# Performance work log

Hardware: AMD Instinct MI355X
Metric: run time of the kernel (lower is better)

## Reference

```python
import jax, jax.numpy as jnp
from jax import lax
import numpy as np

CLASS_NUMBER = 19
REGION_RADIUS = 1
KERNEL = 2 * REGION_RADIUS + 1  # 3
IMAGE_TOPK = 256
EPS = 1e-6


def setup_inputs() -> dict:
    key = jax.random.key(0)
    # softmax-like probabilities over classes
    raw = jax.random.uniform(key, (4, CLASS_NUMBER, 512, 1024), dtype=jnp.float32)
    logit = raw / jnp.sum(raw, axis=1, keepdims=True)
    return {"logit": logit}


def _box_sum(x):
    # kxk box sum with zero padding (SAME for odd kernel == pad=radius)
    return lax.reduce_window(x, jnp.float32(0), lax.add,
                             (1, 1, KERNEL, KERNEL), (1, 1, 1, 1), 'SAME')


def reference(logit):
    B, C, H, W = logit.shape
    logC = jnp.log(jnp.float32(C))

    # region uncertainty: normalized entropy, then avg-pool (count_include_pad)
    entropy = jnp.sum(-logit * jnp.log(logit + EPS), axis=1, keepdims=True) / logC
    region_uncertainty = _box_sum(entropy) / (KERNEL * KERNEL)  # [B,1,H,W]

    # region impurity: argmax -> one-hot -> depthwise box-sum (ones kernel)
    predict = jnp.argmax(logit, axis=1)                       # [B,H,W]
    one_hot = jax.nn.one_hot(predict, C, axis=1, dtype=logit.dtype)  # [B,C,H,W]
    summary = _box_sum(one_hot)                               # [B,C,H,W]
    count = jnp.sum(summary, axis=1, keepdims=True)           # [B,1,H,W]
    dist = summary / count
    region_impurity = jnp.sum(-dist * jnp.log(dist + EPS), axis=1, keepdims=True) / logC

    score = region_uncertainty * region_impurity              # [B,1,H,W]

    # per-image score: sum of top-k region scores
    flat = score.reshape(B, H * W)
    topk_vals, _ = lax.top_k(flat, IMAGE_TOPK)
    image_score = jnp.sum(topk_vals, axis=1)                  # [B]
    return image_score
```

## Files before the change

kernel.cpp:

```cpp
#include <hip/hip_runtime.h>
#include <cstdint>
#include <cstddef>

#define BB 4
#define CC 19
#define HH 512
#define WW 1024
#define HW (HH*WW)
#define HW4 (HW/4)
#define BHW (BB*HW)
#define KTOP 256
#define EPSF 1e-6f
#define NB1 8192
#define SEG 128
#define LOGC 2.9444389791664403f

__device__ __forceinline__ unsigned int sortable(float x) {
    unsigned int u = __float_as_uint(x);
    return (u & 0x80000000u) ? ~u : (u | 0x80000000u);
}
__device__ __forceinline__ float unsortable(unsigned int K) {
    unsigned int u = (K & 0x80000000u) ? (K & 0x7FFFFFFFu) : ~K;
    return __uint_as_float(u);
}

__global__ __launch_bounds__(256) void k_ent(const float4* __restrict__ logit,
                                             float4* __restrict__ ent,
                                             uchar4* __restrict__ pred,
                                             unsigned int* __restrict__ histz) {
    int idx = blockIdx.x * 256 + threadIdx.x;
    if (idx < 65536) histz[idx] = 0;
    int b = idx >> 17;
    int q = idx & (HW4 - 1);
    const float4* base = logit + (size_t)b * CC * HW4 + q;
    float e0 = 0.f, e1 = 0.f, e2 = 0.f, e3 = 0.f;
    float m0 = -1.f, m1 = -1.f, m2 = -1.f, m3 = -1.f;
    int a0 = 0, a1 = 0, a2 = 0, a3 = 0;
#pragma unroll
    for (int c = 0; c < CC; ++c) {
        float4 p = base[(size_t)c * HW4];
        e0 -= p.x * __logf(p.x + EPSF); if (p.x > m0) { m0 = p.x; a0 = c; }
        e1 -= p.y * __logf(p.y + EPSF); if (p.y > m1) { m1 = p.y; a1 = c; }
        e2 -= p.z * __logf(p.z + EPSF); if (p.z > m2) { m2 = p.z; a2 = c; }
        e3 -= p.w * __logf(p.w + EPSF); if (p.w > m3) { m3 = p.w; a3 = c; }
    }
    ent[idx] = make_float4(e0, e1, e2, e3);
    pred[idx] = make_uchar4((unsigned char)a0, (unsigned char)a1,
                            (unsigned char)a2, (unsigned char)a3);
}

__global__ __launch_bounds__(256) void k_score_hist(const float* __restrict__ ent,
                                                    const unsigned char* __restrict__ pred,
                                                    float* __restrict__ score,
                                                    unsigned int* __restrict__ hist1) {
    __shared__ unsigned int lh[NB1];
    int b = blockIdx.x >> 7;
    int seg = blockIdx.x & (SEG - 1);
    for (int i = threadIdx.x; i < NB1; i += 256) lh[i] = 0;
    __syncthreads();
    const float* eb = ent + (size_t)b * HW;
    const unsigned char* pb = pred + (size_t)b * HW;
    int base = seg * (HW / SEG);

    for (int it = 0; it < 16; ++it) {
        int hw = base + it * 256 + threadIdx.x;
        int h = hw >> 10;
        int w = hw & (WW - 1);

        float es = 0.f;
        int cls[9];
        int nv = 0;
#pragma unroll
        for (int i = 0; i < 9; ++i) {
            int dh = i / 3 - 1, dw = i % 3 - 1;
            int hh = h + dh, ww = w + dw;
            bool ok = (hh >= 0) & (hh < HH) & (ww >= 0) & (ww < WW);
            int o = ok ? ((hh << 10) | ww) : 0;
            es += ok ? eb[o] : 0.f;
            cls[i] = ok ? (int)pb[o] : 255;
            nv += ok ? 1 : 0;
        }
        float inv = 1.f / (float)nv;
        float imp = 0.f;
#pragma unroll
        for (int i = 0; i < 9; ++i) {
            if (cls[i] == 255) continue;
            int cnt = 0;
            bool first = true;
#pragma unroll
            for (int j = 0; j < 9; ++j) {
                cnt += (cls[j] == cls[i]) ? 1 : 0;
                if (j < i && cls[j] == cls[i]) first = false;
            }
            if (first) {
                float d = (float)cnt * inv;
                imp -= d * __logf(d + EPSF);
            }
        }
        float v = (es * (1.f / (9.f * LOGC))) * (imp * (1.f / LOGC));
        score[(size_t)b * HW + hw] = v;
        atomicAdd(&lh[sortable(v) >> 19], 1u);
    }
    __syncthreads();
    unsigned int* hb = hist1 + (size_t)b * NB1;
    for (int i = threadIdx.x; i < NB1; i += 256) {
        unsigned int c = lh[i];
        if (c) atomicAdd(&hb[i], c);
    }
}

__device__ __forceinline__ void select_bin(const unsigned int* __restrict__ hb,
                                           int rem, int* bin_out, int* rem_out) {
    __shared__ unsigned int cs[256];
    __shared__ unsigned int bs[32];
    __shared__ int s_chunk, s_bin, s_rem;
    int t = threadIdx.x;
    unsigned int s = 0;
    for (int i = 0; i < 32; ++i) s += hb[t * 32 + i];
    cs[t] = s;
    __syncthreads();
    for (int d = 1; d < 256; d <<= 1) {
        unsigned int v = (t + d < 256) ? cs[t + d] : 0;
        __syncthreads();
        cs[t] += v;
        __syncthreads();
    }
    unsigned int St = cs[t];
    unsigned int St1 = (t < 255) ? cs[t + 1] : 0;
    if ((int)St >= rem && (t == 255 || (int)St1 < rem)) {
        s_chunk = t;
        s_rem = rem - (int)St1;
    }
    __syncthreads();
    int chunk = s_chunk;
    int rem2 = s_rem;
    if (t < 32) bs[t] = hb[chunk * 32 + t];
    __syncthreads();
    for (int d = 1; d < 32; d <<= 1) {
        unsigned int v = (t < 32 && t + d < 32) ? bs[t + d] : 0;
        __syncthreads();
        if (t < 32) bs[t] += v;
        __syncthreads();
    }
    if (t < 32) {
        unsigned int Sb = bs[t];
        unsigned int Sb1 = (t < 31) ? bs[t + 1] : 0;
        if ((int)Sb >= rem2 && (t == 31 || (int)Sb1 < rem2)) {
            s_bin = chunk * 32 + t;
            s_rem = rem2 - (int)Sb1;
        }
    }
    __syncthreads();
    *bin_out = s_bin;
    *rem_out = s_rem;
}

__global__ __launch_bounds__(256) void k_scan1(const unsigned int* __restrict__ hist1,
                                               unsigned int* __restrict__ T1,
                                               int* __restrict__ r1) {
    int b = blockIdx.x;
    int bin, rem;
    select_bin(hist1 + (size_t)b * NB1, KTOP, &bin, &rem);
    if (threadIdx.x == 0) { T1[b] = (unsigned int)bin; r1[b] = rem; }
}

__global__ __launch_bounds__(256) void k_hist2(const float4* __restrict__ score,
                                               const unsigned int* __restrict__ T1,
                                               unsigned int* __restrict__ hist2) {
    __shared__ unsigned int lh[NB1];
    int b = blockIdx.x >> 7;
    int seg = blockIdx.x & (SEG - 1);
    for (int i = threadIdx.x; i < NB1; i += 256) lh[i] = 0;
    __syncthreads();
    unsigned int t1 = T1[b];
    const float4* p = score + ((size_t)b * HW + (size_t)seg * (HW / SEG)) / 4;
    for (int i = threadIdx.x; i < (HW / SEG) / 4; i += 256) {
        float4 v = p[i];
        unsigned int k0 = sortable(v.x), k1 = sortable(v.y);
        unsigned int k2 = sortable(v.z), k3 = sortable(v.w);
        if ((k0 >> 19) == t1) atomicAdd(&lh[(k0 >> 6) & 0x1FFFu], 1u);
        if ((k1 >> 19) == t1) atomicAdd(&lh[(k1 >> 6) & 0x1FFFu], 1u);
        if ((k2 >> 19) == t1) atomicAdd(&lh[(k2 >> 6) & 0x1FFFu], 1u);
        if ((k3 >> 19) == t1) atomicAdd(&lh[(k3 >> 6) & 0x1FFFu], 1u);
    }
    __syncthreads();
    unsigned int* hb = hist2 + (size_t)b * NB1;
    for (int i = threadIdx.x; i < NB1; i += 256) {
        unsigned int c = lh[i];
        if (c) atomicAdd(&hb[i], c);
    }
}

__global__ __launch_bounds__(256) void k_scan2(const unsigned int* __restrict__ hist2,
                                               const unsigned int* __restrict__ T1,
                                               const int* __restrict__ r1,
                                               unsigned int* __restrict__ Kthr,
                                               float* __restrict__ out) {
    int b = blockIdx.x;
    int bin, rem;
    select_bin(hist2 + (size_t)b * NB1, r1[b], &bin, &rem);
    if (threadIdx.x == 0) {
        unsigned int K = (T1[b] << 19) | ((unsigned int)bin << 6);
        Kthr[b] = K;
        out[b] = unsortable(K) * (float)rem;
    }
}

__global__ __launch_bounds__(256) void k_sum(const float* __restrict__ score,
                                             const unsigned int* __restrict__ Kthr,
                                             float* __restrict__ out) {
    int idx = blockIdx.x * 256 + threadIdx.x;
    int b = idx >> 19;
    float v = score[idx];
    unsigned int key = sortable(v);
    if ((key & ~63u) > Kthr[b]) atomicAdd(&out[b], v);
}

extern "C" void kernel_launch(void* const* d_in, const int* in_sizes, int n_in,
                              void* d_out, int out_size, void* d_ws, size_t ws_size,
                              hipStream_t stream) {
    const float* logit = (const float*)d_in[0];
    float* out = (float*)d_out;
    char* ws = (char*)d_ws;

    float*         ent   = (float*)(ws);
    unsigned char* pred  = (unsigned char*)(ws + 8388608);
    float*         score = (float*)(ws + 10485760);
    unsigned int*  hist1 = (unsigned int*)(ws + 18874368);
    unsigned int*  hist2 = (unsigned int*)(ws + 19005440);
    char*          scal  = ws + 19136512;
    unsigned int*  T1    = (unsigned int*)(scal);
    int*           r1    = (int*)(scal + 16);
    unsigned int*  Kthr  = (unsigned int*)(scal + 32);

    k_ent<<<BHW / 4 / 256, 256, 0, stream>>>((const float4*)logit, (float4*)ent,
                                             (uchar4*)pred, hist1 );
    k_score_hist<<<BB * SEG, 256, 0, stream>>>(ent, pred, score, hist1);
    k_scan1<<<BB, 256, 0, stream>>>(hist1, T1, r1);
    k_hist2<<<BB * SEG, 256, 0, stream>>>((const float4*)score, T1, hist2);
    k_scan2<<<BB, 256, 0, stream>>>(hist2, T1, r1, Kthr, out);
    k_sum<<<BHW / 256, 256, 0, stream>>>(score, Kthr, out);
}
```

Before: 294.5 us.

## Fold histogram scans into last-block-done epilogues and vectorize threshold sum

```diff
diff --git a/kernel.cpp b/kernel.cpp
--- a/kernel.cpp
+++ b/kernel.cpp
@@ -24,12 +24,59 @@
     return __uint_as_float(u);
 }
 
+__device__ __forceinline__ void select_bin_lds(const unsigned int* __restrict__ lh,
+                                               int rem, int* bin_out, int* rem_out) {
+    __shared__ unsigned int cs[256];
+    __shared__ unsigned int bs[32];
+    __shared__ int s_chunk, s_bin, s_rem;
+    int t = threadIdx.x;
+    unsigned int s = 0;
+#pragma unroll 8
+    for (int i = 0; i < 32; ++i) s += lh[t * 32 + i];
+    cs[t] = s;
+    __syncthreads();
+    for (int d = 1; d < 256; d <<= 1) {
+        unsigned int v = (t + d < 256) ? cs[t + d] : 0;
+        __syncthreads();
+        cs[t] += v;
+        __syncthreads();
+    }
+    unsigned int St = cs[t];
+    unsigned int St1 = (t < 255) ? cs[t + 1] : 0;
+    if ((int)St >= rem && (t == 255 || (int)St1 < rem)) {
+        s_chunk = t;
+        s_rem = rem - (int)St1;
+    }
+    __syncthreads();
+    int chunk = s_chunk;
+    int rem2 = s_rem;
+    if (t < 32) bs[t] = lh[chunk * 32 + t];
+    __syncthreads();
+    for (int d = 1; d < 32; d <<= 1) {
+        unsigned int v = (t < 32 && t + d < 32) ? bs[t + d] : 0;
+        __syncthreads();
+        if (t < 32) bs[t] += v;
+        __syncthreads();
+    }
+    if (t < 32) {
+        unsigned int Sb = bs[t];
+        unsigned int Sb1 = (t < 31) ? bs[t + 1] : 0;
+        if ((int)Sb >= rem2 && (t == 31 || (int)Sb1 < rem2)) {
+            s_bin = chunk * 32 + t;
+            s_rem = rem2 - (int)Sb1;
+        }
+    }
+    __syncthreads();
+    *bin_out = s_bin;
+    *rem_out = s_rem;
+}
+
 __global__ __launch_bounds__(256) void k_ent(const float4* __restrict__ logit,
                                              float4* __restrict__ ent,
                                              uchar4* __restrict__ pred,
                                              unsigned int* __restrict__ histz) {
     int idx = blockIdx.x * 256 + threadIdx.x;
-    if (idx < 65536) histz[idx] = 0;
+    if (idx < 65568) histz[idx] = 0;
     int b = idx >> 17;
     int q = idx & (HW4 - 1);
     const float4* base = logit + (size_t)b * CC * HW4 + q;
@@ -52,8 +99,12 @@
 __global__ __launch_bounds__(256) void k_score_hist(const float* __restrict__ ent,
                                                     const unsigned char* __restrict__ pred,
                                                     float* __restrict__ score,
-                                                    unsigned int* __restrict__ hist1) {
+                                                    unsigned int* __restrict__ hist1,
+                                                    unsigned int* __restrict__ done1,
+                                                    unsigned int* __restrict__ T1,
+                                                    int* __restrict__ r1) {
     __shared__ unsigned int lh[NB1];
+    __shared__ unsigned int s_flag;
     int b = blockIdx.x >> 7;
     int seg = blockIdx.x & (SEG - 1);
     for (int i = threadIdx.x; i < NB1; i += 256) lh[i] = 0;
@@ -107,67 +158,31 @@
         unsigned int c = lh[i];
         if (c) atomicAdd(&hb[i], c);
     }
-}
-
-__device__ __forceinline__ void select_bin(const unsigned int* __restrict__ hb,
-                                           int rem, int* bin_out, int* rem_out) {
-    __shared__ unsigned int cs[256];
-    __shared__ unsigned int bs[32];
-    __shared__ int s_chunk, s_bin, s_rem;
-    int t = threadIdx.x;
-    unsigned int s = 0;
-    for (int i = 0; i < 32; ++i) s += hb[t * 32 + i];
-    cs[t] = s;
-    __syncthreads();
-    for (int d = 1; d < 256; d <<= 1) {
-        unsigned int v = (t + d < 256) ? cs[t + d] : 0;
-        __syncthreads();
-        cs[t] += v;
-        __syncthreads();
-    }
-    unsigned int St = cs[t];
-    unsigned int St1 = (t < 255) ? cs[t + 1] : 0;
-    if ((int)St >= rem && (t == 255 || (int)St1 < rem)) {
-        s_chunk = t;
-        s_rem = rem - (int)St1;
-    }
-    __syncthreads();
-    int chunk = s_chunk;
-    int rem2 = s_rem;
-    if (t < 32) bs[t] = hb[chunk * 32 + t];
-    __syncthreads();
-    for (int d = 1; d < 32; d <<= 1) {
-        unsigned int v = (t < 32 && t + d < 32) ? bs[t + d] : 0;
-        __syncthreads();
-        if (t < 32) bs[t] += v;
-        __syncthreads();
-    }
-    if (t < 32) {
-        unsigned int Sb = bs[t];
-        unsigned int Sb1 = (t < 31) ? bs[t + 1] : 0;
-        if ((int)Sb >= rem2 && (t == 31 || (int)Sb1 < rem2)) {
-            s_bin = chunk * 32 + t;
-            s_rem = rem2 - (int)Sb1;
-        }
-    }
-    __syncthreads();
-    *bin_out = s_bin;
-    *rem_out = s_rem;
-}
-
-__global__ __launch_bounds__(256) void k_scan1(const unsigned int* __restrict__ hist1,
-                                               unsigned int* __restrict__ T1,
-                                               int* __restrict__ r1) {
-    int b = blockIdx.x;
-    int bin, rem;
-    select_bin(hist1 + (size_t)b * NB1, KTOP, &bin, &rem);
-    if (threadIdx.x == 0) { T1[b] = (unsigned int)bin; r1[b] = rem; }
+    __syncthreads();
+    if (threadIdx.x == 0) {
+        __threadfence();
+        unsigned int old = atomicAdd(&done1[b], 1u);
+        s_flag = (old == SEG - 1) ? 1u : 0u;
+    }
+    __syncthreads();
+    if (s_flag) {
+        for (int i = threadIdx.x; i < NB1; i += 256) lh[i] = atomicAdd(&hb[i], 0u);
+        __syncthreads();
+        int bin, rem;
+        select_bin_lds(lh, KTOP, &bin, &rem);
+        if (threadIdx.x == 0) { T1[b] = (unsigned int)bin; r1[b] = rem; }
+    }
 }
 
 __global__ __launch_bounds__(256) void k_hist2(const float4* __restrict__ score,
                                                const unsigned int* __restrict__ T1,
-                                               unsigned int* __restrict__ hist2) {
+                                               const int* __restrict__ r1,
+                                               unsigned int* __restrict__ hist2,
+                                               unsigned int* __restrict__ done2,
+                                               unsigned int* __restrict__ Kthr,
+                                               float* __restrict__ out) {
     __shared__ unsigned int lh[NB1];
+    __shared__ unsigned int s_flag;
     int b = blockIdx.x >> 7;
     int seg = blockIdx.x & (SEG - 1);
     for (int i = threadIdx.x; i < NB1; i += 256) lh[i] = 0;
@@ -189,31 +204,37 @@
         unsigned int c = lh[i];
         if (c) atomicAdd(&hb[i], c);
     }
-}
-
-__global__ __launch_bounds__(256) void k_scan2(const unsigned int* __restrict__ hist2,
-                                               const unsigned int* __restrict__ T1,
-                                               const int* __restrict__ r1,
-                                               unsigned int* __restrict__ Kthr,
-                                               float* __restrict__ out) {
-    int b = blockIdx.x;
-    int bin, rem;
-    select_bin(hist2 + (size_t)b * NB1, r1[b], &bin, &rem);
+    __syncthreads();
     if (threadIdx.x == 0) {
-        unsigned int K = (T1[b] << 19) | ((unsigned int)bin << 6);
-        Kthr[b] = K;
-        out[b] = unsortable(K) * (float)rem;
-    }
-}
-
-__global__ __launch_bounds__(256) void k_sum(const float* __restrict__ score,
+        __threadfence();
+        unsigned int old = atomicAdd(&done2[b], 1u);
+        s_flag = (old == SEG - 1) ? 1u : 0u;
+    }
+    __syncthreads();
+    if (s_flag) {
+        for (int i = threadIdx.x; i < NB1; i += 256) lh[i] = atomicAdd(&hb[i], 0u);
+        __syncthreads();
+        int bin, rem;
+        select_bin_lds(lh, r1[b], &bin, &rem);
+        if (threadIdx.x == 0) {
+            unsigned int K = (t1 << 19) | ((unsigned int)bin << 6);
+            Kthr[b] = K;
+            out[b] = unsortable(K) * (float)rem;
+        }
+    }
+}
+
+__global__ __launch_bounds__(256) void k_sum(const float4* __restrict__ score,
                                              const unsigned int* __restrict__ Kthr,
                                              float* __restrict__ out) {
     int idx = blockIdx.x * 256 + threadIdx.x;
-    int b = idx >> 19;
-    float v = score[idx];
-    unsigned int key = sortable(v);
-    if ((key & ~63u) > Kthr[b]) atomicAdd(&out[b], v);
+    int b = idx >> 17;
+    unsigned int Kb = Kthr[b];
+    float4 v = score[idx];
+    if ((sortable(v.x) & ~63u) > Kb) atomicAdd(&out[b], v.x);
+    if ((sortable(v.y) & ~63u) > Kb) atomicAdd(&out[b], v.y);
+    if ((sortable(v.z) & ~63u) > Kb) atomicAdd(&out[b], v.z);
+    if ((sortable(v.w) & ~63u) > Kb) atomicAdd(&out[b], v.w);
 }
 
 extern "C" void kernel_launch(void* const* d_in, const int* in_sizes, int n_in,
@@ -226,18 +247,19 @@
     float*         ent   = (float*)(ws);
     unsigned char* pred  = (unsigned char*)(ws + 8388608);
     float*         score = (float*)(ws + 10485760);
-    unsigned int*  hist1 = (unsigned int*)(ws + 18874368);
-    unsigned int*  hist2 = (unsigned int*)(ws + 19005440);
-    char*          scal  = ws + 19136512;
-    unsigned int*  T1    = (unsigned int*)(scal);
-    int*           r1    = (int*)(scal + 16);
-    unsigned int*  Kthr  = (unsigned int*)(scal + 32);
+    unsigned int*  histb = (unsigned int*)(ws + 18874368);
+    unsigned int*  hist1 = histb;
+    unsigned int*  hist2 = histb + 32768;
+    unsigned int*  T1    = histb + 65536;
+    int*           r1    = (int*)(histb + 65540);
+    unsigned int*  Kthr  = histb + 65544;
+    unsigned int*  done1 = histb + 65548;
+    unsigned int*  done2 = histb + 65552;
 
     k_ent<<<BHW / 4 / 256, 256, 0, stream>>>((const float4*)logit, (float4*)ent,
-                                             (uchar4*)pred, hist1 );
-    k_score_hist<<<BB * SEG, 256, 0, stream>>>(ent, pred, score, hist1);
-    k_scan1<<<BB, 256, 0, stream>>>(hist1, T1, r1);
-    k_hist2<<<BB * SEG, 256, 0, stream>>>((const float4*)score, T1, hist2);
-    k_scan2<<<BB, 256, 0, stream>>>(hist2, T1, r1, Kthr, out);
-    k_sum<<<BHW / 256, 256, 0, stream>>>(score, Kthr, out);
-}
+                                             (uchar4*)pred, histb );
+    k_score_hist<<<BB * SEG, 256, 0, stream>>>(ent, pred, score, hist1, done1, T1, r1);
+    k_hist2<<<BB * SEG, 256, 0, stream>>>((const float4*)score, T1, r1,
+                                          hist2, done2, Kthr, out);
+    k_sum<<<BHW / 4 / 256, 256, 0, stream>>>((const float4*)score, Kthr, out);
+}
```

After: 319.4 us. 8.4% more time.

## Fold top-k summation into second histogram pass and simplify impurity math

Applied to the files above, without the earlier changes.

```diff
diff --git a/kernel.cpp b/kernel.cpp
--- a/kernel.cpp
+++ b/kernel.cpp
@@ -27,9 +27,11 @@
 __global__ __launch_bounds__(256) void k_ent(const float4* __restrict__ logit,
                                              float4* __restrict__ ent,
                                              uchar4* __restrict__ pred,
-                                             unsigned int* __restrict__ histz) {
+                                             unsigned int* __restrict__ histz,
+                                             float* __restrict__ outz) {
     int idx = blockIdx.x * 256 + threadIdx.x;
-    if (idx < 65536) histz[idx] = 0;
+    if (idx < 98312) histz[idx] = 0;
+    if (idx < BB) outz[idx] = 0.f;
     int b = idx >> 17;
     int q = idx & (HW4 - 1);
     const float4* base = logit + (size_t)b * CC * HW4 + q;
@@ -81,22 +83,16 @@
             nv += ok ? 1 : 0;
         }
         float inv = 1.f / (float)nv;
-        float imp = 0.f;
+        float lsum = 0.f;
 #pragma unroll
         for (int i = 0; i < 9; ++i) {
-            if (cls[i] == 255) continue;
             int cnt = 0;
-            bool first = true;
-#pragma unroll
-            for (int j = 0; j < 9; ++j) {
-                cnt += (cls[j] == cls[i]) ? 1 : 0;
-                if (j < i && cls[j] == cls[i]) first = false;
-            }
-            if (first) {
-                float d = (float)cnt * inv;
-                imp -= d * __logf(d + EPSF);
-            }
-        }
+#pragma unroll
+            for (int j = 0; j < 9; ++j) cnt += (cls[j] == cls[i]) ? 1 : 0;
+            float lg = __logf((float)cnt * inv + EPSF);
+            lsum += (cls[i] != 255) ? lg : 0.f;
+        }
+        float imp = -inv * lsum;
         float v = (es * (1.f / (9.f * LOGC))) * (imp * (1.f / LOGC));
         score[(size_t)b * HW + hw] = v;
         atomicAdd(&lh[sortable(v) >> 19], 1u);
@@ -116,6 +112,7 @@
     __shared__ int s_chunk, s_bin, s_rem;
     int t = threadIdx.x;
     unsigned int s = 0;
+#pragma unroll 8
     for (int i = 0; i < 32; ++i) s += hb[t * 32 + i];
     cs[t] = s;
     __syncthreads();
@@ -166,54 +163,74 @@
 
 __global__ __launch_bounds__(256) void k_hist2(const float4* __restrict__ score,
                                                const unsigned int* __restrict__ T1,
-                                               unsigned int* __restrict__ hist2) {
+                                               unsigned int* __restrict__ hist2,
+                                               float* __restrict__ hsum,
+                                               float* __restrict__ out) {
     __shared__ unsigned int lh[NB1];
+    __shared__ float ls[NB1];
+    __shared__ float red[4];
     int b = blockIdx.x >> 7;
     int seg = blockIdx.x & (SEG - 1);
-    for (int i = threadIdx.x; i < NB1; i += 256) lh[i] = 0;
+    for (int i = threadIdx.x; i < NB1; i += 256) { lh[i] = 0; ls[i] = 0.f; }
     __syncthreads();
     unsigned int t1 = T1[b];
     const float4* p = score + ((size_t)b * HW + (size_t)seg * (HW / SEG)) / 4;
+    float sa = 0.f;
     for (int i = threadIdx.x; i < (HW / SEG) / 4; i += 256) {
         float4 v = p[i];
-        unsigned int k0 = sortable(v.x), k1 = sortable(v.y);
-        unsigned int k2 = sortable(v.z), k3 = sortable(v.w);
-        if ((k0 >> 19) == t1) atomicAdd(&lh[(k0 >> 6) & 0x1FFFu], 1u);
-        if ((k1 >> 19) == t1) atomicAdd(&lh[(k1 >> 6) & 0x1FFFu], 1u);
-        if ((k2 >> 19) == t1) atomicAdd(&lh[(k2 >> 6) & 0x1FFFu], 1u);
-        if ((k3 >> 19) == t1) atomicAdd(&lh[(k3 >> 6) & 0x1FFFu], 1u);
+        float vv[4] = {v.x, v.y, v.z, v.w};
+#pragma unroll
+        for (int q = 0; q < 4; ++q) {
+            unsigned int k = sortable(vv[q]);
+            unsigned int cb = k >> 19;
+            if (cb > t1) sa += vv[q];
+            else if (cb == t1) {
+                int sub = (k >> 6) & 0x1FFF;
+                atomicAdd(&lh[sub], 1u);
+                atomicAdd(&ls[sub], vv[q]);
+            }
+        }
     }
     __syncthreads();
     unsigned int* hb = hist2 + (size_t)b * NB1;
+    float* sb = hsum + (size_t)b * NB1;
     for (int i = threadIdx.x; i < NB1; i += 256) {
         unsigned int c = lh[i];
-        if (c) atomicAdd(&hb[i], c);
+        if (c) { atomicAdd(&hb[i], c); atomicAdd(&sb[i], ls[i]); }
+    }
+#pragma unroll
+    for (int d = 32; d; d >>= 1) sa += __shfl_down(sa, d);
+    if ((threadIdx.x & 63) == 0) red[threadIdx.x >> 6] = sa;
+    __syncthreads();
+    if (threadIdx.x == 0) {
+        float tt = red[0] + red[1] + red[2] + red[3];
+        if (tt != 0.f) atomicAdd(&out[b], tt);
     }
 }
 
 __global__ __launch_bounds__(256) void k_scan2(const unsigned int* __restrict__ hist2,
+                                               const float* __restrict__ hsum,
                                                const unsigned int* __restrict__ T1,
                                                const int* __restrict__ r1,
-                                               unsigned int* __restrict__ Kthr,
                                                float* __restrict__ out) {
     int b = blockIdx.x;
     int bin, rem;
     select_bin(hist2 + (size_t)b * NB1, r1[b], &bin, &rem);
-    if (threadIdx.x == 0) {
+    __shared__ float rs[256];
+    int t = threadIdx.x;
+    const float* sb = hsum + (size_t)b * NB1;
+    float s = 0.f;
+    for (int i = t; i < NB1; i += 256) if (i > bin) s += sb[i];
+    rs[t] = s;
+    __syncthreads();
+    for (int d = 128; d; d >>= 1) {
+        if (t < d) rs[t] += rs[t + d];
+        __syncthreads();
+    }
+    if (t == 0) {
         unsigned int K = (T1[b] << 19) | ((unsigned int)bin << 6);
-        Kthr[b] = K;
-        out[b] = unsortable(K) * (float)rem;
-    }
-}
-
-__global__ __launch_bounds__(256) void k_sum(const float* __restrict__ score,
-                                             const unsigned int* __restrict__ Kthr,
-                                             float* __restrict__ out) {
-    int idx = blockIdx.x * 256 + threadIdx.x;
-    int b = idx >> 19;
-    float v = score[idx];
-    unsigned int key = sortable(v);
-    if ((key & ~63u) > Kthr[b]) atomicAdd(&out[b], v);
+        out[b] += rs[0] + unsortable(K) * (float)rem;
+    }
 }
 
 extern "C" void kernel_launch(void* const* d_in, const int* in_sizes, int n_in,
@@ -226,18 +243,17 @@
     float*         ent   = (float*)(ws);
     unsigned char* pred  = (unsigned char*)(ws + 8388608);
     float*         score = (float*)(ws + 10485760);
-    unsigned int*  hist1 = (unsigned int*)(ws + 18874368);
-    unsigned int*  hist2 = (unsigned int*)(ws + 19005440);
-    char*          scal  = ws + 19136512;
-    unsigned int*  T1    = (unsigned int*)(scal);
-    int*           r1    = (int*)(scal + 16);
-    unsigned int*  Kthr  = (unsigned int*)(scal + 32);
+    unsigned int*  histb = (unsigned int*)(ws + 18874368);
+    unsigned int*  hist1 = histb;
+    unsigned int*  hist2 = histb + 32768;
+    float*         hsum  = (float*)(histb + 65536);
+    unsigned int*  T1    = histb + 98304;
+    int*           r1    = (int*)(histb + 98308);
 
     k_ent<<<BHW / 4 / 256, 256, 0, stream>>>((const float4*)logit, (float4*)ent,
-                                             (uchar4*)pred, hist1 );
+                                             (uchar4*)pred, histb, out);
     k_score_hist<<<BB * SEG, 256, 0, stream>>>(ent, pred, score, hist1);
     k_scan1<<<BB, 256, 0, stream>>>(hist1, T1, r1);
-    k_hist2<<<BB * SEG, 256, 0, stream>>>((const float4*)score, T1, hist2);
-    k_scan2<<<BB, 256, 0, stream>>>(hist2, T1, r1, Kthr, out);
-    k_sum<<<BHW / 256, 256, 0, stream>>>(score, Kthr, out);
-}
+    k_hist2<<<BB * SEG, 256, 0, stream>>>((const float4*)score, T1, hist2, hsum, out);
+    k_scan2<<<BB, 256, 0, stream>>>(hist2, hsum, T1, r1, out);
+}
```

Result: no change. 298.3 us (+1.3%).
